# Kernel optimization log

Measured on AMD Instinct MI355X. Metric: run time of the kernel, lower is better.

The kernel has to match this reference:

```python
import jax, jax.numpy as jnp
import numpy as np
from jax.scipy.linalg import solve_triangular, cho_solve

K_SPARSE = 5
COMMIT = 0.25
EPS = 1e-10


def batch_omp(X, D, K):
    """Batched Orthogonal Matching Pursuit.
    X: [C, M] signals (columns). D: [C, N] L2-normalized dictionary.
    Returns support [M, K] (int32) and coefficients [M, K] in selection order.
    """
    G = D.T @ D                    # [N, N] Gram matrix
    h_bar = (D.T @ X).T            # [M, N] correlations
    M, N = h_bar.shape
    h = h_bar
    mask = jnp.ones((M, N), dtype=bool)
    gamma = jnp.zeros_like(h_bar)
    L = jnp.ones((M, 1, 1), dtype=X.dtype)
    rows = jnp.arange(M)
    I = None
    for k in range(1, K + 1):  # K is small and static -> unrolled
        idx = jnp.argmax(jnp.abs(h) * mask, axis=1)          # [M]
        mask = mask.at[rows, idx].set(False)
        if k > 1:
            G_col = G[I, idx[:, None]]                        # [M, k-1]
            w = solve_triangular(L, G_col[..., None], lower=True)[..., 0]  # [M, k-1]
            corner = jnp.sqrt(jnp.clip(1.0 - jnp.sum(w * w, axis=1), 1e-12))  # [M]
            top = jnp.concatenate([L, jnp.zeros((M, k - 1, 1), X.dtype)], axis=2)
            bot = jnp.concatenate([w[:, None, :], corner[:, None, None]], axis=2)
            L = jnp.concatenate([top, bot], axis=1)           # [M, k, k]
            I = jnp.concatenate([I, idx[:, None]], axis=1)
        else:
            I = idx[:, None]
        h_sel = h_bar[rows[:, None], I]                       # [M, k]
        gamma_sel = cho_solve((L, True), h_sel[..., None])[..., 0]  # [M, k]
        gamma = gamma.at[rows[:, None], I].set(gamma_sel)
        # beta = gamma_sel @ G[I]  -> residual update over all atoms
        beta = jnp.einsum('mk,mkn->mn', gamma_sel, G[I])      # [M, N]
        h = h_bar - beta
    coeffs = gamma[rows[:, None], I]                          # [M, K]
    return I, coeffs


def setup_inputs() -> dict:
    key = jax.random.key(0)
    k1, k2 = jax.random.split(key)
    z_e = jax.random.normal(k1, (8, 64, 64, 64), dtype=jnp.float32)        # [B, C, H, W]
    dictionary = jax.random.normal(k2, (64, 512), dtype=jnp.float32)       # [C, N]
    return {"z_e": z_e, "dictionary": dictionary}


def reference(z_e, dictionary):
    B, C, H, W = z_e.shape
    # [B,C,H,W] -> [C, B*H*W] column signals
    signals = z_e.transpose(0, 2, 3, 1).reshape(-1, C).T
    # L2-normalize dictionary columns (F.normalize with dim=0)
    norms = jnp.linalg.norm(dictionary, axis=0, keepdims=True)
    Dn = dictionary / jnp.maximum(norms, EPS)
    # OMP runs under no_grad in the original
    support, coeffs = batch_omp(jax.lax.stop_gradient(signals),
                                jax.lax.stop_gradient(Dn), K_SPARSE)
    # reconstruct: sum_k coeff_k * atom_k (gradient flows through Dn)
    atoms = Dn.T[support]                                     # [M, K, C]
    recon = jnp.einsum('mkc,mk->mc', atoms, coeffs)           # [M, C]
    z_dl = recon.reshape(B, H, W, C).transpose(0, 3, 1, 2)    # [B, C, H, W]
    dl_latent_loss = jnp.mean((z_dl - jax.lax.stop_gradient(z_e)) ** 2)
    e_latent_loss = jnp.mean((jax.lax.stop_gradient(z_dl) - z_e) ** 2)
    loss = dl_latent_loss + COMMIT * e_latent_loss
    z_dl_ste = z_e + jax.lax.stop_gradient(z_dl - z_e)        # straight-through
    return (z_dl_ste, loss,
            support.reshape(B, H, W, K_SPARSE),
            coeffs.reshape(B, H, W, K_SPARSE))
```

## Files before the change

### kernel.cpp

```cpp
#include <hip/hip_runtime.h>

#define NC 64
#define NA 512
#define KS 5

#define WS_DN   0
#define WS_DNT  32768
#define WS_G    65536
#define WS_ACCF 327680

#define OUT_LOSS 2097152
#define OUT_SUP  2097153
#define OUT_COF  2260993

__global__ void norm_kernel(const float* __restrict__ D, float* __restrict__ Dn,
                            float* __restrict__ DnT) {
  int n = blockIdx.x * 64 + threadIdx.x;
  float s = 0.f;
  for (int c = 0; c < NC; ++c) {
    float v = D[c * NA + n];
    s += v * v;
  }
  float den = fmaxf(sqrtf(s), 1e-10f);
  for (int c = 0; c < NC; ++c) {
    float v = D[c * NA + n] / den;
    Dn[c * NA + n]  = v;
    DnT[n * NC + c] = v;
  }
}

__global__ void gram_kernel(const float* __restrict__ Dn,
                            float* __restrict__ G, double* __restrict__ accum) {
  __shared__ float col[NC];
  int i = blockIdx.x, t = threadIdx.x;
  if (t < NC) col[t] = Dn[t * NA + i];
  if (i == 0 && t == 0) *accum = 0.0;
  __syncthreads();
  float s = 0.f;
#pragma unroll
  for (int c = 0; c < NC; ++c) s += col[c] * Dn[c * NA + t];
  G[(size_t)i * NA + t] = s;
}

template<int KK>
__device__ __forceinline__ void omp_stepH(
    const int hl, const float* __restrict__ G,
    const float* __restrict__ parkS,
    float (&h16)[16], unsigned &msk, int (&I)[KS],
    float (&Lo)[10], float (&rd)[KS], float (&gam)[KS]) {
  float bv = -1.f; int bn = 0;
#pragma unroll
  for (int s = 0; s < 16; ++s) {
    int a = ((s >> 1) << 6) + 2 * hl + (s & 1);
    float v = ((msk >> s) & 1u) ? fabsf(h16[s]) : 0.f;
    if (v > bv) { bv = v; bn = a; }
  }
#pragma unroll
  for (int off = 1; off < 32; off <<= 1) {
    float ov = __shfl_xor(bv, off);
    int   on = __shfl_xor(bn, off);
    if (ov > bv || (ov == bv && on < bn)) { bv = ov; bn = on; }
  }
  const int idx = bn;
  if (((idx & 63) >> 1) == hl)
    msk &= ~(1u << (((idx >> 6) << 1) | (idx & 1)));
  I[KK] = idx;

  if constexpr (KK == 0) {
    rd[0] = 1.f;
  } else {
    float Gc[KK], w_[KK];
#pragma unroll
    for (int j = 0; j < KK; ++j) Gc[j] = G[(size_t)I[j] * NA + idx];
#pragma unroll
    for (int i = 0; i < KK; ++i) {
      float ssum = Gc[i];
#pragma unroll
      for (int j = 0; j < i; ++j) ssum -= Lo[i*(i-1)/2 + j] * w_[j];
      w_[i] = ssum * rd[i];
    }
    float ww = 0.f;
#pragma unroll
    for (int i = 0; i < KK; ++i) ww += w_[i] * w_[i];
    float corner = sqrtf(fmaxf(1.f - ww, 1e-12f));
#pragma unroll
    for (int j = 0; j < KK; ++j) Lo[KK*(KK-1)/2 + j] = w_[j];
    rd[KK] = 1.f / corner;
  }

  float y[KK + 1];
#pragma unroll
  for (int i = 0; i <= KK; ++i) {
    float b_ = parkS[I[i]];
#pragma unroll
    for (int j = 0; j < i; ++j) b_ -= Lo[i*(i-1)/2 + j] * y[j];
    y[i] = b_ * rd[i];
  }
#pragma unroll
  for (int i = KK; i >= 0; --i) {
    float g_ = y[i];
#pragma unroll
    for (int j = i + 1; j <= KK; ++j) g_ -= Lo[j*(j-1)/2 + i] * gam[j];
    gam[i] = g_ * rd[i];
  }

  if constexpr (KK < 4) {
    const float2* pk2 = (const float2*)parkS;
#pragma unroll
    for (int i = 0; i < 8; ++i) {
      float2 hv = pk2[(i << 5) + hl];
      h16[i * 2] = hv.x; h16[i * 2 + 1] = hv.y;
    }
#pragma unroll
    for (int j = 0; j <= KK; ++j) {
      const float2* g2 = (const float2*)(G + (size_t)I[j] * NA);
      const float gj = gam[j];
#pragma unroll
      for (int i = 0; i < 8; ++i) {
        float2 g = g2[(i << 5) + hl];
        h16[i * 2]     -= gj * g.x;
        h16[i * 2 + 1] -= gj * g.y;
      }
    }
  }
}

__global__ __launch_bounds__(256, 2) void omp_kernel(
    const float* __restrict__ z, const float* __restrict__ Dn,
    const float* __restrict__ DnT, const float* __restrict__ G,
    float* __restrict__ out, double* __restrict__ accum) {
  __shared__ __align__(16) float buf[8 * NA];
  __shared__ float xsz[8 * NC];
  __shared__ double wsq[8];
  const int t = threadIdx.x, lane = t & 63, wv = t >> 6;
  const int hl = lane & 31;
  const int m0 = blockIdx.x * 8;
  const int bh = m0 >> 6, b = bh >> 6, h = bh & 63, w0 = m0 & 63;
  const size_t zbase = (size_t)b * 262144 + (size_t)h * 64 + w0;

  const float4* D4 = (const float4*)Dn;
  float4 r0 = D4[t], r1 = D4[256 + t], r2 = D4[512 + t], r3 = D4[768 + t];

  for (int j = t; j < 8 * NC; j += 256) {
    int c = j >> 3, s = j & 7;
    xsz[s * NC + c] = z[zbase + (size_t)c * 4096 + s];
  }
  __syncthreads();
  const float xf0 = xsz[(wv * 2 + 0) * NC + lane];
  const float xf1 = xsz[(wv * 2 + 1) * NC + lane];
  const int sig = wv * 2 + (lane >> 5);
  const float xfa = xsz[sig * NC + hl];
  const float xfb = xsz[sig * NC + hl + 32];

  {
    float acc[2][8];
#pragma unroll
    for (int si = 0; si < 2; ++si)
#pragma unroll
      for (int i = 0; i < 8; ++i) acc[si][i] = 0.f;

    float4* st4 = (float4*)buf;
    for (int ch = 0; ch < 8; ++ch) {
      if (ch) __syncthreads();
      st4[t] = r0; st4[256 + t] = r1; st4[512 + t] = r2; st4[768 + t] = r3;
      __syncthreads();
      if (ch < 7) {
        const float4* Dx = D4 + (ch + 1) * 1024;
        r0 = Dx[t]; r1 = Dx[256 + t]; r2 = Dx[512 + t]; r3 = Dx[768 + t];
      }
#pragma unroll
      for (int c8 = 0; c8 < 8; ++c8) {
        const int c = ch * 8 + c8;
        const float x0 = __shfl(xf0, c);
        const float x1 = __shfl(xf1, c);
        const float2* row2 = (const float2*)(buf + c8 * NA);
#pragma unroll
        for (int i = 0; i < 4; ++i) {
          float2 dv = row2[(i << 6) + lane];
          acc[0][i * 2] += x0 * dv.x; acc[0][i * 2 + 1] += x0 * dv.y;
          acc[1][i * 2] += x1 * dv.x; acc[1][i * 2 + 1] += x1 * dv.y;
        }
      }
    }
    __syncthreads();
    float2* park2 = (float2*)buf;
#pragma unroll
    for (int si = 0; si < 2; ++si)
#pragma unroll
      for (int i = 0; i < 4; ++i) {
        float2 v; v.x = acc[si][i * 2]; v.y = acc[si][i * 2 + 1];
        park2[(size_t)(wv * 2 + si) * 256 + (i << 6) + lane] = v;
      }
  }

  const float* parkS = buf + (size_t)sig * NA;
  float h16[16];
  {
    const float2* pk2 = (const float2*)parkS;
#pragma unroll
    for (int i = 0; i < 8; ++i) {
      float2 hv = pk2[(i << 5) + hl];
      h16[i * 2] = hv.x; h16[i * 2 + 1] = hv.y;
    }
  }
  unsigned msk = 0xFFFFu;
  int I[KS];
  float Lo[10], rd[KS], gam[KS];

  omp_stepH<0>(hl, G, parkS, h16, msk, I, Lo, rd, gam);
  omp_stepH<1>(hl, G, parkS, h16, msk, I, Lo, rd, gam);
  omp_stepH<2>(hl, G, parkS, h16, msk, I, Lo, rd, gam);
  omp_stepH<3>(hl, G, parkS, h16, msk, I, Lo, rd, gam);
  omp_stepH<4>(hl, G, parkS, h16, msk, I, Lo, rd, gam);

  float rrA = 0.f, rrB = 0.f;
#pragma unroll
  for (int j = 0; j < KS; ++j) {
    const float* dr = DnT + (size_t)I[j] * NC;
    rrA += gam[j] * dr[hl];
    rrB += gam[j] * dr[hl + 32];
  }
  const float dA = rrA - xfa, dB = rrB - xfb;
  xsz[hl * 8 + sig]        = xfa + dA;
  xsz[(hl + 32) * 8 + sig] = xfb + dB;
  double sq = (double)dA * (double)dA + (double)dB * (double)dB;
#pragma unroll
  for (int off = 1; off < 32; off <<= 1) sq += __shfl_xor(sq, off);
  if (hl == 0) wsq[sig] = sq;

  if (hl < KS) {
    int   iv = I[0];
    float gv = gam[0];
    if (hl == 1) { iv = I[1]; gv = gam[1]; }
    if (hl == 2) { iv = I[2]; gv = gam[2]; }
    if (hl == 3) { iv = I[3]; gv = gam[3]; }
    if (hl == 4) { iv = I[4]; gv = gam[4]; }
    const int m = m0 + sig;
    out[OUT_SUP + (size_t)m * KS + hl] = (float)iv;
    out[OUT_COF + (size_t)m * KS + hl] = gv;
  }

  __syncthreads();
  for (int j = t; j < 8 * NC; j += 256) {
    int c = j >> 3, s = j & 7;
    out[zbase + (size_t)c * 4096 + s] = xsz[j];
  }
  if (t == 0) {
    double ssum = 0.0;
#pragma unroll
    for (int i = 0; i < 8; ++i) ssum += wsq[i];
    atomicAdd(accum, ssum);
  }
}

__global__ void final_kernel(const double* __restrict__ accum, float* __restrict__ out) {
  double mse = *accum / 2097152.0;
  out[OUT_LOSS] = (float)(mse + 0.25 * mse);
}

extern "C" void kernel_launch(void* const* d_in, const int* in_sizes, int n_in,
                              void* d_out, int out_size, void* d_ws, size_t ws_size,
                              hipStream_t stream) {
  const float* z_e = (const float*)d_in[0];
  const float* dic = (const float*)d_in[1];
  float* out = (float*)d_out;
  float* ws = (float*)d_ws;
  float* Dn   = ws + WS_DN;
  float* DnT  = ws + WS_DNT;
  float* G    = ws + WS_G;
  double* accu = (double*)(ws + WS_ACCF);

  hipLaunchKernelGGL(norm_kernel,  dim3(8),    dim3(64),  0, stream, dic, Dn, DnT);
  hipLaunchKernelGGL(gram_kernel,  dim3(NA),   dim3(NA),  0, stream, Dn, G, accu);
  hipLaunchKernelGGL(omp_kernel,   dim3(4096), dim3(256), 0, stream,
                     z_e, Dn, DnT, G, out, accu);
  hipLaunchKernelGGL(final_kernel, dim3(1),    dim3(1),   0, stream, accu, out);
}
```

Before: 171.6 us.

## Compute correlations from global memory directly and widen OMP lane layout to float4

```diff
diff --git a/kernel.cpp b/kernel.cpp
--- a/kernel.cpp
+++ b/kernel.cpp
@@ -51,7 +51,7 @@
   float bv = -1.f; int bn = 0;
 #pragma unroll
   for (int s = 0; s < 16; ++s) {
-    int a = ((s >> 1) << 6) + 2 * hl + (s & 1);
+    int a = ((s >> 2) << 7) + 4 * hl + (s & 3);
     float v = ((msk >> s) & 1u) ? fabsf(h16[s]) : 0.f;
     if (v > bv) { bv = v; bn = a; }
   }
@@ -62,9 +62,18 @@
     if (ov > bv || (ov == bv && on < bn)) { bv = ov; bn = on; }
   }
   const int idx = bn;
-  if (((idx & 63) >> 1) == hl)
-    msk &= ~(1u << (((idx >> 6) << 1) | (idx & 1)));
+  if (((idx & 127) >> 2) == hl)
+    msk &= ~(1u << (((idx >> 7) << 2) | (idx & 3)));
   I[KK] = idx;
+
+  if constexpr (KK < 4) {
+    const float4* pk4 = (const float4*)parkS;
+#pragma unroll
+    for (int i = 0; i < 4; ++i) {
+      float4 hv = pk4[(i << 5) + hl];
+      h16[i*4+0] = hv.x; h16[i*4+1] = hv.y; h16[i*4+2] = hv.z; h16[i*4+3] = hv.w;
+    }
+  }
 
   if constexpr (KK == 0) {
     rd[0] = 1.f;
@@ -88,38 +97,31 @@
     rd[KK] = 1.f / corner;
   }
 
-  float y[KK + 1];
 #pragma unroll
   for (int i = 0; i <= KK; ++i) {
     float b_ = parkS[I[i]];
 #pragma unroll
-    for (int j = 0; j < i; ++j) b_ -= Lo[i*(i-1)/2 + j] * y[j];
-    y[i] = b_ * rd[i];
+    for (int j = 0; j < i; ++j) b_ -= Lo[i*(i-1)/2 + j] * gam[j];
+    gam[i] = b_ * rd[i];
   }
 #pragma unroll
   for (int i = KK; i >= 0; --i) {
-    float g_ = y[i];
+    float g_ = gam[i];
 #pragma unroll
     for (int j = i + 1; j <= KK; ++j) g_ -= Lo[j*(j-1)/2 + i] * gam[j];
     gam[i] = g_ * rd[i];
   }
 
   if constexpr (KK < 4) {
-    const float2* pk2 = (const float2*)parkS;
-#pragma unroll
-    for (int i = 0; i < 8; ++i) {
-      float2 hv = pk2[(i << 5) + hl];
-      h16[i * 2] = hv.x; h16[i * 2 + 1] = hv.y;
-    }
 #pragma unroll
     for (int j = 0; j <= KK; ++j) {
-      const float2* g2 = (const float2*)(G + (size_t)I[j] * NA);
+      const float4* g4 = (const float4*)(G + (size_t)I[j] * NA);
       const float gj = gam[j];
 #pragma unroll
-      for (int i = 0; i < 8; ++i) {
-        float2 g = g2[(i << 5) + hl];
-        h16[i * 2]     -= gj * g.x;
-        h16[i * 2 + 1] -= gj * g.y;
+      for (int i = 0; i < 4; ++i) {
+        float4 g = g4[(i << 5) + hl];
+        h16[i*4+0] -= gj * g.x; h16[i*4+1] -= gj * g.y;
+        h16[i*4+2] -= gj * g.z; h16[i*4+3] -= gj * g.w;
       }
     }
   }
@@ -129,7 +131,7 @@
     const float* __restrict__ z, const float* __restrict__ Dn,
     const float* __restrict__ DnT, const float* __restrict__ G,
     float* __restrict__ out, double* __restrict__ accum) {
-  __shared__ __align__(16) float buf[8 * NA];
+  __shared__ __align__(16) float park[8 * NA];
   __shared__ float xsz[8 * NC];
   __shared__ double wsq[8];
   const int t = threadIdx.x, lane = t & 63, wv = t >> 6;
@@ -138,69 +140,50 @@
   const int bh = m0 >> 6, b = bh >> 6, h = bh & 63, w0 = m0 & 63;
   const size_t zbase = (size_t)b * 262144 + (size_t)h * 64 + w0;
 
-  const float4* D4 = (const float4*)Dn;
-  float4 r0 = D4[t], r1 = D4[256 + t], r2 = D4[512 + t], r3 = D4[768 + t];
-
   for (int j = t; j < 8 * NC; j += 256) {
     int c = j >> 3, s = j & 7;
     xsz[s * NC + c] = z[zbase + (size_t)c * 4096 + s];
   }
   __syncthreads();
-  const float xf0 = xsz[(wv * 2 + 0) * NC + lane];
-  const float xf1 = xsz[(wv * 2 + 1) * NC + lane];
   const int sig = wv * 2 + (lane >> 5);
-  const float xfa = xsz[sig * NC + hl];
-  const float xfb = xsz[sig * NC + hl + 32];
+  const float2 xf2 = *(const float2*)&xsz[sig * NC + 2 * hl];
 
   {
-    float acc[2][8];
-#pragma unroll
-    for (int si = 0; si < 2; ++si)
-#pragma unroll
-      for (int i = 0; i < 8; ++i) acc[si][i] = 0.f;
-
-    float4* st4 = (float4*)buf;
-    for (int ch = 0; ch < 8; ++ch) {
-      if (ch) __syncthreads();
-      st4[t] = r0; st4[256 + t] = r1; st4[512 + t] = r2; st4[768 + t] = r3;
-      __syncthreads();
-      if (ch < 7) {
-        const float4* Dx = D4 + (ch + 1) * 1024;
-        r0 = Dx[t]; r1 = Dx[256 + t]; r2 = Dx[512 + t]; r3 = Dx[768 + t];
-      }
-#pragma unroll
-      for (int c8 = 0; c8 < 8; ++c8) {
-        const int c = ch * 8 + c8;
-        const float x0 = __shfl(xf0, c);
-        const float x1 = __shfl(xf1, c);
-        const float2* row2 = (const float2*)(buf + c8 * NA);
-#pragma unroll
-        for (int i = 0; i < 4; ++i) {
-          float2 dv = row2[(i << 6) + lane];
-          acc[0][i * 2] += x0 * dv.x; acc[0][i * 2 + 1] += x0 * dv.y;
-          acc[1][i * 2] += x1 * dv.x; acc[1][i * 2 + 1] += x1 * dv.y;
-        }
-      }
-    }
-    __syncthreads();
-    float2* park2 = (float2*)buf;
-#pragma unroll
-    for (int si = 0; si < 2; ++si)
-#pragma unroll
-      for (int i = 0; i < 4; ++i) {
-        float2 v; v.x = acc[si][i * 2]; v.y = acc[si][i * 2 + 1];
-        park2[(size_t)(wv * 2 + si) * 256 + (i << 6) + lane] = v;
-      }
-  }
-
-  const float* parkS = buf + (size_t)sig * NA;
+    float acc[8][2];
+#pragma unroll
+    for (int s = 0; s < 8; ++s) { acc[s][0] = 0.f; acc[s][1] = 0.f; }
+
+    const float2* Dn2 = (const float2*)Dn + (wv << 6) + lane;
+    const float4* zp4 = (const float4*)(z + zbase);
+#pragma unroll 8
+    for (int c = 0; c < 64; ++c) {
+      float2 dv = Dn2[c << 8];
+      float4 xa = zp4[(c << 10)];
+      float4 xb = zp4[(c << 10) + 1];
+      acc[0][0] += xa.x * dv.x; acc[0][1] += xa.x * dv.y;
+      acc[1][0] += xa.y * dv.x; acc[1][1] += xa.y * dv.y;
+      acc[2][0] += xa.z * dv.x; acc[2][1] += xa.z * dv.y;
+      acc[3][0] += xa.w * dv.x; acc[3][1] += xa.w * dv.y;
+      acc[4][0] += xb.x * dv.x; acc[4][1] += xb.x * dv.y;
+      acc[5][0] += xb.y * dv.x; acc[5][1] += xb.y * dv.y;
+      acc[6][0] += xb.z * dv.x; acc[6][1] += xb.z * dv.y;
+      acc[7][0] += xb.w * dv.x; acc[7][1] += xb.w * dv.y;
+    }
+    float2* park2 = (float2*)park;
+#pragma unroll
+    for (int s = 0; s < 8; ++s)
+      park2[(s << 8) + (wv << 6) + lane] = make_float2(acc[s][0], acc[s][1]);
+  }
+  __syncthreads();
+
+  const float* parkS = park + (size_t)sig * NA;
   float h16[16];
   {
-    const float2* pk2 = (const float2*)parkS;
-#pragma unroll
-    for (int i = 0; i < 8; ++i) {
-      float2 hv = pk2[(i << 5) + hl];
-      h16[i * 2] = hv.x; h16[i * 2 + 1] = hv.y;
+    const float4* pk4 = (const float4*)parkS;
+#pragma unroll
+    for (int i = 0; i < 4; ++i) {
+      float4 hv = pk4[(i << 5) + hl];
+      h16[i*4+0] = hv.x; h16[i*4+1] = hv.y; h16[i*4+2] = hv.z; h16[i*4+3] = hv.w;
     }
   }
   unsigned msk = 0xFFFFu;
@@ -216,13 +199,13 @@
   float rrA = 0.f, rrB = 0.f;
 #pragma unroll
   for (int j = 0; j < KS; ++j) {
-    const float* dr = DnT + (size_t)I[j] * NC;
-    rrA += gam[j] * dr[hl];
-    rrB += gam[j] * dr[hl + 32];
-  }
-  const float dA = rrA - xfa, dB = rrB - xfb;
-  xsz[hl * 8 + sig]        = xfa + dA;
-  xsz[(hl + 32) * 8 + sig] = xfb + dB;
+    const float2 dvv = ((const float2*)(DnT + (size_t)I[j] * NC))[hl];
+    rrA += gam[j] * dvv.x;
+    rrB += gam[j] * dvv.y;
+  }
+  const float dA = rrA - xf2.x, dB = rrB - xf2.y;
+  xsz[(2 * hl) * 8 + sig]     = xf2.x + dA;
+  xsz[(2 * hl + 1) * 8 + sig] = xf2.y + dB;
   double sq = (double)dA * (double)dA + (double)dB * (double)dB;
 #pragma unroll
   for (int off = 1; off < 32; off <<= 1) sq += __shfl_xor(sq, off);
```

Result: faster. 152.3 us (-11.3%).
